# Optimization experiments

Measured on AMD Instinct MI355X. Metric: run time of the kernel, lower is better.

The kernel has to match this reference:

```python
import jax, jax.numpy as jnp
import numpy as np

E, C, H, I = 8, 1024, 2048, 4096  # experts, capacity, hidden, intermediate


def setup_inputs() -> dict:
    key = jax.random.key(0)
    k1, k2, k3 = jax.random.split(key, 3)
    hidden_states = jax.random.normal(k1, (E, C, H), dtype=jnp.float32)
    # fused gate/up projection weights per expert: [E, H, 2*I]
    w_gate_up = jax.random.normal(k2, (E, H, 2 * I), dtype=jnp.float32) * (1.0 / np.sqrt(H))
    # down projection weights per expert: [E, I, H]
    w_down = jax.random.normal(k3, (E, I, H), dtype=jnp.float32) * (1.0 / np.sqrt(I))
    return {"hidden_states": hidden_states, "w_gate_up": w_gate_up, "w_down": w_down}


def reference(hidden_states, w_gate_up, w_down):
    # Batched per-expert gate/up GEMM: (E,C,H) @ (E,H,2I) -> (E,C,2I)
    gate_up = jnp.einsum("ech,ehf->ecf", hidden_states, w_gate_up)
    gate, up = jnp.split(gate_up, 2, axis=-1)  # each (E,C,I)
    act = jax.nn.silu(gate) * up  # GLU activation
    # Batched per-expert down GEMM: (E,C,I) @ (E,I,H) -> (E,C,H)
    out = jnp.einsum("eci,eih->ech", act, w_down)
    return out
```

## Files before the change

### kernel.cpp

```cpp
#include <hip/hip_runtime.h>
#include <stdint.h>


#define E_  8
#define C_  1024
#define H_  2048
#define I_  4096
#define N1_ 8192

typedef __bf16 bf16x8 __attribute__((ext_vector_type(8)));
typedef float  f32x4  __attribute__((ext_vector_type(4)));

typedef __attribute__((address_space(3))) unsigned       lds_uint;
typedef const __attribute__((address_space(1))) unsigned glob_uint;

__device__ __forceinline__ void gload_lds16(const void* g, void* l) {
    __builtin_amdgcn_global_load_lds((glob_uint*)g, (lds_uint*)l, 16, 0, 0);
}

__device__ __forceinline__ unsigned short f2bf(float f) {
    union { float f; unsigned u; } v; v.f = f;
    unsigned u = v.u;
    return (unsigned short)((u + 0x7FFFu + ((u >> 16) & 1u)) >> 16);
}

__device__ __forceinline__ unsigned swz8(unsigned row) {
    return ((row ^ (row >> 2)) & 7u) << 4;
}

#define SBAR0 __builtin_amdgcn_sched_barrier(0)
#define MFMA_ __builtin_amdgcn_mfma_f32_16x16x32_bf16

__global__ void k_convert(const float* __restrict__ src,
                          unsigned short* __restrict__ dst, int n8) {
    int idx = blockIdx.x * blockDim.x + threadIdx.x;
    int stride = gridDim.x * blockDim.x;
    for (int i = idx; i < n8; i += stride) {
        const float4* s = reinterpret_cast<const float4*>(src + (size_t)i * 8);
        float4 a = s[0], b = s[1];
        ushort4 lo, hi;
        lo.x = f2bf(a.x); lo.y = f2bf(a.y); lo.z = f2bf(a.z); lo.w = f2bf(a.w);
        hi.x = f2bf(b.x); hi.y = f2bf(b.y); hi.z = f2bf(b.z); hi.w = f2bf(b.w);
        ushort4* d = reinterpret_cast<ushort4*>(dst + (size_t)i * 8);
        d[0] = lo; d[1] = hi;
    }
}

template<int LD>
__device__ __forceinline__ void stageA(const char* __restrict__ gtile,
                                       char* ldst, int j, int tid, int wave) {
    unsigned p   = (unsigned)(j * 8192 + tid * 16);
    unsigned row = p >> 7;
    unsigned kb  = (p & 127u) ^ swz8(row);
    const char* gp = gtile + (size_t)row * LD + kb;
    void* lp = ldst + j * 8192 + wave * 1024;
    gload_lds16(gp, lp);
}

__device__ __forceinline__ const bf16x8* frag128(const char* tile, int row, int kb) {
    unsigned phys = (unsigned)(row * 128) + ((unsigned)kb ^ swz8((unsigned)row));
    return reinterpret_cast<const bf16x8*>(tile + phys);
}

template<int LDB>
__device__ __forceinline__ void loadB8(const char* __restrict__ gcol, int kt,
                                       float4 (&bk)[8]) {
    const char* p = gcol + (size_t)(kt * 64) * LDB;
    #pragma unroll
    for (int i = 0; i < 8; ++i)
        bk[i] = *reinterpret_cast<const float4*>(p + (size_t)i * LDB);
}

__device__ __forceinline__ void cvtWriteB(char* bB, const float4 (&bk)[8],
                                          int rg, int kg8) {
    const float* f = reinterpret_cast<const float*>(&bk[0]);
    #pragma unroll
    for (int j = 0; j < 4; ++j) {
        unsigned u[4];
        #pragma unroll
        for (int p2 = 0; p2 < 4; ++p2) {
            float lo = f[(2 * p2) * 4 + j];
            float hi = f[(2 * p2 + 1) * 4 + j];
            asm("v_cvt_pk_bf16_f32 %0, %1, %2" : "=v"(u[p2]) : "v"(lo), "v"(hi));
        }
        unsigned q = (unsigned)(rg * 4 + j);
        unsigned phys = q * 128 + (((unsigned)kg8 * 16) ^ swz8(q));
        *reinterpret_cast<uint4*>(bB + phys) = make_uint4(u[0], u[1], u[2], u[3]);
    }
}

template<int LDA, int LDB, int NT, int BMG, int BNG, int MODE>
__global__ __launch_bounds__(512, 2) void k_gemm_f(
    const unsigned short* __restrict__ A,
    const float* __restrict__ B,
    void* __restrict__ Cout,
    size_t sA, size_t sB) {
    __shared__ char lds[131072];

    const int tid = threadIdx.x, lane = tid & 63, wave = tid >> 6;
    const int wm = wave >> 2, wn = wave & 3;
    const int kg = lane >> 4, r = lane & 15;
    const int rg = tid & 63, kg8 = tid >> 6;

    unsigned flat = blockIdx.x;
    unsigned cpx = gridDim.x >> 3;
    unsigned nid = (flat & 7u) * cpx + (flat >> 3);
    const int bm = nid % BMG;
    const int bn = (nid / BMG) % BNG;
    const int e  = nid / (BMG * BNG);

    const char* gA = (const char*)(A + sA * e) + (size_t)(bm * 256) * LDA;
    size_t colstart;
    if constexpr (MODE == 0)
        colstart = (size_t)(bn * 128 + ((rg >> 4) & 3) * 32 + ((rg >> 2) & 1) * 16
                            + (rg & 3) * 4)
                 + (((rg >> 3) & 1) ? (size_t)I_ : (size_t)0);
    else
        colstart = (size_t)(bn * 256 + rg * 4);
    const char* gBcol = (const char*)B + sB * e + colstart * 4
                      + (size_t)kg8 * 8 * LDB;

    float4 bk[8];

    loadB8<LDB>(gBcol, 0, bk);
    SBAR0;
    asm volatile("s_waitcnt vmcnt(0)" ::: "memory");
    SBAR0;
    cvtWriteB(lds + 32768, bk, rg, kg8);
    SBAR0;
    stageA<LDA>(gA, lds, 0, tid, wave);
    stageA<LDA>(gA, lds, 1, tid, wave);
    stageA<LDA>(gA, lds, 2, tid, wave);
    stageA<LDA>(gA, lds, 3, tid, wave);
    SBAR0;
    loadB8<LDB>(gBcol, 1, bk);
    SBAR0;
    asm volatile("s_waitcnt vmcnt(8)" ::: "memory");
    asm volatile("s_waitcnt lgkmcnt(0)" ::: "memory");
    SBAR0;
    __builtin_amdgcn_s_barrier();
    SBAR0;

    f32x4 acc[8][4] = {};

    for (int t = 0; t < NT; ++t) {
        const char* Ab = lds + (t & 1) * 65536;
        const char* Bb = Ab + 32768;
        char* nA = lds + ((t + 1) & 1) * 65536;
        char* nB = nA + 32768;
        const char* gAn = gA + (size_t)(t + 1) * 128;
        const bool hs1 = (t + 1) < NT, hs2 = (t + 2) < NT;

        bf16x8 af[8], b0[2], bg[2];

        if (hs1) {
            asm volatile("s_waitcnt vmcnt(0)" ::: "memory");
            SBAR0;
            cvtWriteB(nB, bk, rg, kg8);
            SBAR0;
            stageA<LDA>(gAn, nA, 0, tid, wave);
            stageA<LDA>(gAn, nA, 1, tid, wave);
            stageA<LDA>(gAn, nA, 2, tid, wave);
            stageA<LDA>(gAn, nA, 3, tid, wave);
            SBAR0;
            if (hs2) { loadB8<LDB>(gBcol, t + 2, bk); SBAR0; }
        }

        #pragma unroll
        for (int m = 0; m < 8; ++m)
            af[m] = *frag128(Ab, wm * 128 + m * 16 + r, kg * 16);
        #pragma unroll
        for (int n = 0; n < 2; ++n)
            b0[n] = *frag128(Bb, wn * 64 + n * 16 + r, kg * 16);
        asm volatile("s_waitcnt lgkmcnt(0)" ::: "memory");
        SBAR0;
        __builtin_amdgcn_s_setprio(1);
        #pragma unroll
        for (int m = 0; m < 8; ++m) {
            acc[m][0] = MFMA_(af[m], b0[0], acc[m][0], 0, 0, 0);
            acc[m][1] = MFMA_(af[m], b0[1], acc[m][1], 0, 0, 0);
        }
        __builtin_amdgcn_s_setprio(0);
        SBAR0;

        #pragma unroll
        for (int n = 0; n < 2; ++n)
            bg[n] = *frag128(Bb, wn * 64 + 32 + n * 16 + r, kg * 16);
        asm volatile("s_waitcnt lgkmcnt(0)" ::: "memory");
        SBAR0;
        __builtin_amdgcn_s_setprio(1);
        #pragma unroll
        for (int m = 0; m < 8; ++m) {
            acc[m][2] = MFMA_(af[m], bg[0], acc[m][2], 0, 0, 0);
            acc[m][3] = MFMA_(af[m], bg[1], acc[m][3], 0, 0, 0);
        }
        __builtin_amdgcn_s_setprio(0);
        SBAR0;

        #pragma unroll
        for (int m = 0; m < 8; ++m)
            af[m] = *frag128(Ab, wm * 128 + m * 16 + r, 64 + kg * 16);
        #pragma unroll
        for (int n = 0; n < 2; ++n)
            b0[n] = *frag128(Bb, wn * 64 + n * 16 + r, 64 + kg * 16);
        asm volatile("s_waitcnt lgkmcnt(0)" ::: "memory");
        SBAR0;
        __builtin_amdgcn_s_setprio(1);
        #pragma unroll
        for (int m = 0; m < 8; ++m) {
            acc[m][0] = MFMA_(af[m], b0[0], acc[m][0], 0, 0, 0);
            acc[m][1] = MFMA_(af[m], b0[1], acc[m][1], 0, 0, 0);
        }
        __builtin_amdgcn_s_setprio(0);
        SBAR0;

        #pragma unroll
        for (int n = 0; n < 2; ++n)
            bg[n] = *frag128(Bb, wn * 64 + 32 + n * 16 + r, 64 + kg * 16);
        asm volatile("s_waitcnt lgkmcnt(0)" ::: "memory");
        SBAR0;
        __builtin_amdgcn_s_setprio(1);
        #pragma unroll
        for (int m = 0; m < 8; ++m) {
            acc[m][2] = MFMA_(af[m], bg[0], acc[m][2], 0, 0, 0);
            acc[m][3] = MFMA_(af[m], bg[1], acc[m][3], 0, 0, 0);
        }
        __builtin_amdgcn_s_setprio(0);
        SBAR0;

        if (hs1) {
            SBAR0;
            if (hs2) asm volatile("s_waitcnt vmcnt(8)" ::: "memory");
            else     asm volatile("s_waitcnt vmcnt(0)" ::: "memory");
            asm volatile("s_waitcnt lgkmcnt(0)" ::: "memory");
            SBAR0;
            __builtin_amdgcn_s_barrier();
            SBAR0;
        }
    }

    const int row0 = bm * 256 + wm * 128 + kg * 4;
    if constexpr (MODE == 0) {
        unsigned short* act = (unsigned short*)Cout + (size_t)e * C_ * I_;
        const int col0 = bn * 128 + wn * 32 + r;
        #pragma unroll
        for (int m = 0; m < 8; ++m)
            #pragma unroll
            for (int n = 0; n < 2; ++n)
                #pragma unroll
                for (int j = 0; j < 4; ++j) {
                    float g = acc[m][n][j], u = acc[m][n + 2][j];
                    float s = g / (1.0f + __expf(-g)) * u;
                    act[(size_t)(row0 + m * 16 + j) * I_ + col0 + n * 16] = f2bf(s);
                }
    } else {
        float* o = (float*)Cout + (size_t)e * C_ * H_;
        const int col0 = bn * 256 + wn * 64 + r;
        #pragma unroll
        for (int m = 0; m < 8; ++m)
            #pragma unroll
            for (int n = 0; n < 4; ++n)
                #pragma unroll
                for (int j = 0; j < 4; ++j)
                    o[(size_t)(row0 + m * 16 + j) * H_ + col0 + n * 16] = acc[m][n][j];
    }
}

extern "C" void kernel_launch(void* const* d_in, const int* in_sizes, int n_in,
                              void* d_out, int out_size, void* d_ws, size_t ws_size,
                              hipStream_t stream) {
    const float* hs  = (const float*)d_in[0];
    const float* wgu = (const float*)d_in[1];
    const float* wd  = (const float*)d_in[2];
    float* out = (float*)d_out;

    char* ws = (char*)d_ws;
    unsigned short* Xbf  = (unsigned short*)(ws);
    unsigned short* actb = (unsigned short*)(ws + 33554432ull);

    k_convert<<<2048, 256, 0, stream>>>(hs, Xbf, E_ * C_ * H_ / 8);

    k_gemm_f<H_ * 2, N1_ * 4, H_ / 64, 4, 32, 0><<<dim3(1024), 512, 0, stream>>>(
        Xbf, wgu, actb, (size_t)C_ * H_, (size_t)H_ * N1_ * 4);

    k_gemm_f<I_ * 2, H_ * 4, I_ / 64, 4, 8, 1><<<dim3(256), 512, 0, stream>>>(
        actb, wd, out, (size_t)C_ * I_, (size_t)I_ * H_ * 4);
}
```

Measured before the change: 474.3 us.

## Switch GEMM inner loop from 16x16x32 to 32x32x16 bf16 MFMA tiles

New measurement: 503.7 us. 1.06x slower.

```diff
diff --git a/kernel.cpp b/kernel.cpp
--- a/kernel.cpp
+++ b/kernel.cpp
@@ -9,7 +9,7 @@
 #define N1_ 8192
 
 typedef __bf16 bf16x8 __attribute__((ext_vector_type(8)));
-typedef float  f32x4  __attribute__((ext_vector_type(4)));
+typedef float  f32x16 __attribute__((ext_vector_type(16)));
 
 typedef __attribute__((address_space(3))) unsigned       lds_uint;
 typedef const __attribute__((address_space(1))) unsigned glob_uint;
@@ -29,7 +29,7 @@
 }
 
 #define SBAR0 __builtin_amdgcn_sched_barrier(0)
-#define MFMA_ __builtin_amdgcn_mfma_f32_16x16x32_bf16
+#define MFMA32_ __builtin_amdgcn_mfma_f32_32x32x16_bf16
 
 __global__ void k_convert(const float* __restrict__ src,
                           unsigned short* __restrict__ dst, int n8) {
@@ -99,7 +99,7 @@
 
     const int tid = threadIdx.x, lane = tid & 63, wave = tid >> 6;
     const int wm = wave >> 2, wn = wave & 3;
-    const int kg = lane >> 4, r = lane & 15;
+    const int l31 = lane & 31, lhi = lane >> 5;
     const int rg = tid & 63, kg8 = tid >> 6;
 
     unsigned flat = blockIdx.x;
@@ -111,12 +111,13 @@
 
     const char* gA = (const char*)(A + sA * e) + (size_t)(bm * 256) * LDA;
     size_t colstart;
-    if constexpr (MODE == 0)
-        colstart = (size_t)(bn * 128 + ((rg >> 4) & 3) * 32 + ((rg >> 2) & 1) * 16
-                            + (rg & 3) * 4)
-                 + (((rg >> 3) & 1) ? (size_t)I_ : (size_t)0);
-    else
+    if constexpr (MODE == 0) {
+        int b = rg >> 3;
+        colstart = (size_t)(bn * 128 + (b >> 1) * 32 + (rg & 7) * 4)
+                 + ((b & 1) ? (size_t)I_ : (size_t)0);
+    } else {
         colstart = (size_t)(bn * 256 + rg * 4);
+    }
     const char* gBcol = (const char*)B + sB * e + colstart * 4
                       + (size_t)kg8 * 8 * LDB;
 
@@ -141,7 +142,7 @@
     __builtin_amdgcn_s_barrier();
     SBAR0;
 
-    f32x4 acc[8][4] = {};
+    f32x16 acc[4][2] = {};
 
     for (int t = 0; t < NT; ++t) {
         const char* Ab = lds + (t & 1) * 65536;
@@ -151,8 +152,6 @@
         const char* gAn = gA + (size_t)(t + 1) * 128;
         const bool hs1 = (t + 1) < NT, hs2 = (t + 2) < NT;
 
-        bf16x8 af[8], b0[2], bg[2];
-
         if (hs1) {
             asm volatile("s_waitcnt vmcnt(0)" ::: "memory");
             SBAR0;
@@ -167,66 +166,33 @@
         }
 
         #pragma unroll
-        for (int m = 0; m < 8; ++m)
-            af[m] = *frag128(Ab, wm * 128 + m * 16 + r, kg * 16);
-        #pragma unroll
-        for (int n = 0; n < 2; ++n)
-            b0[n] = *frag128(Bb, wn * 64 + n * 16 + r, kg * 16);
-        asm volatile("s_waitcnt lgkmcnt(0)" ::: "memory");
-        SBAR0;
-        __builtin_amdgcn_s_setprio(1);
-        #pragma unroll
-        for (int m = 0; m < 8; ++m) {
-            acc[m][0] = MFMA_(af[m], b0[0], acc[m][0], 0, 0, 0);
-            acc[m][1] = MFMA_(af[m], b0[1], acc[m][1], 0, 0, 0);
-        }
-        __builtin_amdgcn_s_setprio(0);
-        SBAR0;
-
-        #pragma unroll
-        for (int n = 0; n < 2; ++n)
-            bg[n] = *frag128(Bb, wn * 64 + 32 + n * 16 + r, kg * 16);
-        asm volatile("s_waitcnt lgkmcnt(0)" ::: "memory");
-        SBAR0;
-        __builtin_amdgcn_s_setprio(1);
-        #pragma unroll
-        for (int m = 0; m < 8; ++m) {
-            acc[m][2] = MFMA_(af[m], bg[0], acc[m][2], 0, 0, 0);
-            acc[m][3] = MFMA_(af[m], bg[1], acc[m][3], 0, 0, 0);
-        }
-        __builtin_amdgcn_s_setprio(0);
-        SBAR0;
-
-        #pragma unroll
-        for (int m = 0; m < 8; ++m)
-            af[m] = *frag128(Ab, wm * 128 + m * 16 + r, 64 + kg * 16);
-        #pragma unroll
-        for (int n = 0; n < 2; ++n)
-            b0[n] = *frag128(Bb, wn * 64 + n * 16 + r, 64 + kg * 16);
-        asm volatile("s_waitcnt lgkmcnt(0)" ::: "memory");
-        SBAR0;
-        __builtin_amdgcn_s_setprio(1);
-        #pragma unroll
-        for (int m = 0; m < 8; ++m) {
-            acc[m][0] = MFMA_(af[m], b0[0], acc[m][0], 0, 0, 0);
-            acc[m][1] = MFMA_(af[m], b0[1], acc[m][1], 0, 0, 0);
-        }
-        __builtin_amdgcn_s_setprio(0);
-        SBAR0;
-
-        #pragma unroll
-        for (int n = 0; n < 2; ++n)
-            bg[n] = *frag128(Bb, wn * 64 + 32 + n * 16 + r, 64 + kg * 16);
-        asm volatile("s_waitcnt lgkmcnt(0)" ::: "memory");
-        SBAR0;
-        __builtin_amdgcn_s_setprio(1);
-        #pragma unroll
-        for (int m = 0; m < 8; ++m) {
-            acc[m][2] = MFMA_(af[m], bg[0], acc[m][2], 0, 0, 0);
-            acc[m][3] = MFMA_(af[m], bg[1], acc[m][3], 0, 0, 0);
-        }
-        __builtin_amdgcn_s_setprio(0);
-        SBAR0;
+        for (int ph = 0; ph < 2; ++ph) {
+            const int kb0 = ph * 64 + lhi * 16;
+            const int kb1 = ph * 64 + 32 + lhi * 16;
+            bf16x8 af[4][2], bf[2][2];
+            #pragma unroll
+            for (int mf = 0; mf < 4; ++mf) {
+                af[mf][0] = *frag128(Ab, wm * 128 + mf * 32 + l31, kb0);
+                af[mf][1] = *frag128(Ab, wm * 128 + mf * 32 + l31, kb1);
+            }
+            #pragma unroll
+            for (int nf = 0; nf < 2; ++nf) {
+                bf[nf][0] = *frag128(Bb, wn * 64 + nf * 32 + l31, kb0);
+                bf[nf][1] = *frag128(Bb, wn * 64 + nf * 32 + l31, kb1);
+            }
+            asm volatile("s_waitcnt lgkmcnt(0)" ::: "memory");
+            SBAR0;
+            __builtin_amdgcn_s_setprio(1);
+            #pragma unroll
+            for (int mf = 0; mf < 4; ++mf)
+                #pragma unroll
+                for (int nf = 0; nf < 2; ++nf) {
+                    acc[mf][nf] = MFMA32_(af[mf][0], bf[nf][0], acc[mf][nf], 0, 0, 0);
+                    acc[mf][nf] = MFMA32_(af[mf][1], bf[nf][1], acc[mf][nf], 0, 0, 0);
+                }
+            __builtin_amdgcn_s_setprio(0);
+            SBAR0;
+        }
 
         if (hs1) {
             SBAR0;
@@ -239,30 +205,35 @@
         }
     }
 
-    const int row0 = bm * 256 + wm * 128 + kg * 4;
     if constexpr (MODE == 0) {
         unsigned short* act = (unsigned short*)Cout + (size_t)e * C_ * I_;
-        const int col0 = bn * 128 + wn * 32 + r;
-        #pragma unroll
-        for (int m = 0; m < 8; ++m)
-            #pragma unroll
-            for (int n = 0; n < 2; ++n)
-                #pragma unroll
-                for (int j = 0; j < 4; ++j) {
-                    float g = acc[m][n][j], u = acc[m][n + 2][j];
-                    float s = g / (1.0f + __expf(-g)) * u;
-                    act[(size_t)(row0 + m * 16 + j) * I_ + col0 + n * 16] = f2bf(s);
-                }
+        const int col = bn * 128 + wn * 32 + l31;
+        #pragma unroll
+        for (int mf = 0; mf < 4; ++mf) {
+            const int rbase = bm * 256 + wm * 128 + mf * 32 + 4 * lhi;
+            #pragma unroll
+            for (int reg = 0; reg < 16; ++reg) {
+                int row = rbase + (reg & 3) + 8 * (reg >> 2);
+                float g = acc[mf][0][reg], u = acc[mf][1][reg];
+                float s = g / (1.0f + __expf(-g)) * u;
+                act[(size_t)row * I_ + col] = f2bf(s);
+            }
+        }
     } else {
         float* o = (float*)Cout + (size_t)e * C_ * H_;
-        const int col0 = bn * 256 + wn * 64 + r;
-        #pragma unroll
-        for (int m = 0; m < 8; ++m)
-            #pragma unroll
-            for (int n = 0; n < 4; ++n)
+        #pragma unroll
+        for (int mf = 0; mf < 4; ++mf) {
+            const int rbase = bm * 256 + wm * 128 + mf * 32 + 4 * lhi;
+            #pragma unroll
+            for (int nf = 0; nf < 2; ++nf) {
+                const int col = bn * 256 + wn * 64 + nf * 32 + l31;
                 #pragma unroll
-                for (int j = 0; j < 4; ++j)
-                    o[(size_t)(row0 + m * 16 + j) * H_ + col0 + n * 16] = acc[m][n][j];
+                for (int reg = 0; reg < 16; ++reg) {
+                    int row = rbase + (reg & 3) + 8 * (reg >> 2);
+                    o[(size_t)row * H_ + col] = acc[mf][nf][reg];
+                }
+            }
+        }
     }
 }
 
```
